# Optimization experiments

Hardware: AMD Instinct MI355X
Metric: run time of the kernel (lower is better)

The kernel has to match this reference:

```python
import jax, jax.numpy as jnp
import numpy as np

N_NODES = 50000
EPS = 1e-12  # F.normalize eps


def _gcn_layer(x, W, b, src, dst):
    # GCNConv(normalize=False): h = x @ W, then sum-aggregate messages from
    # source nodes into target nodes along edge_index, then add bias.
    h = x @ W
    agg = jax.ops.segment_sum(h[src], dst, num_segments=N_NODES)
    out = agg + b
    # F.normalize(p=2, dim=-1) then ReLU
    norm = jnp.linalg.norm(out, axis=-1, keepdims=True)
    out = out / jnp.maximum(norm, EPS)
    return jax.nn.relu(out)


def setup_inputs() -> dict:
    key = jax.random.key(0)
    ks = jax.random.split(key, 8)
    nfeat, nhid, nclass, n_edges = 128, 128, 40, 640000
    x = jax.random.normal(ks[0], (N_NODES, nfeat), dtype=jnp.float32)
    edge_index = jax.random.randint(ks[1], (2, n_edges), 0, N_NODES, dtype=jnp.int64)
    s = 1.0 / np.sqrt(nhid)
    return {
        "x": x,
        "edge_index": edge_index,
        "W1": jax.random.normal(ks[2], (nfeat, nhid), jnp.float32) * s,
        "b1": jnp.zeros((nhid,), jnp.float32),
        "W2": jax.random.normal(ks[3], (nhid, nhid), jnp.float32) * s,
        "b2": jnp.zeros((nhid,), jnp.float32),
        "W3": jax.random.normal(ks[4], (nhid, nhid), jnp.float32) * s,
        "b3": jnp.zeros((nhid,), jnp.float32),
        "W4": jax.random.normal(ks[5], (nhid, nhid), jnp.float32) * s,
        "b4": jnp.zeros((nhid,), jnp.float32),
        "Wl": jax.random.normal(ks[6], (nhid, nclass), jnp.float32) * s,
        "bl": jnp.zeros((nclass,), jnp.float32),
    }


def reference(x, edge_index, W1, b1, W2, b2, W3, b3, W4, b4, Wl, bl):
    src, dst = edge_index[0], edge_index[1]
    x1 = _gcn_layer(x, W1, b1, src, dst)
    x2 = _gcn_layer(x1, W2, b2, src, dst)
    x3 = _gcn_layer(x2, W3, b3, src, dst)
    x4 = _gcn_layer(x3, W4, b4, src, dst)
    logits = x4 @ Wl + bl
    probs = jax.nn.softmax(logits, axis=-1)
    return (logits, probs, x4)
```

## Files before the change

### kernel.cpp

```cpp
#include <hip/hip_runtime.h>
#include <hip/hip_bf16.h>
#include <hip/hip_fp16.h>
#include <math.h>

#define NFEAT 128
#define NCLASS 40

typedef __attribute__((ext_vector_type(8))) short frag_ab;
typedef __attribute__((ext_vector_type(4))) float frag_cd;

static __device__ inline unsigned short f2bf_rne(float f) {
    union { float f; unsigned u; } v;
    v.f = f;
    unsigned r = v.u + 0x7FFFu + ((v.u >> 16) & 1u);
    return (unsigned short)(r >> 16);
}
static __device__ inline float bf2f(unsigned short h) {
    union { unsigned u; float f; } v;
    v.u = ((unsigned)h) << 16;
    return v.f;
}


__global__ __launch_bounds__(256) void prep_kernel(const float* __restrict__ x,
                                                   __half* __restrict__ xh, int xc4,
                                                   int* __restrict__ cnt, int n_nodes,
                                                   const float* __restrict__ W0,
                                                   const float* __restrict__ W1,
                                                   const float* __restrict__ W2,
                                                   const float* __restrict__ W3,
                                                   short* __restrict__ whi,
                                                   short* __restrict__ wlo,
                                                   int convB, int zeroB) {
    int b = blockIdx.x;
    if (b < convB) {
        int i = b * 256 + threadIdx.x;
        if (i < xc4) {
            float4 v = ((const float4*)x)[i];
            ((__half2*)xh)[i * 2 + 0] = __floats2half2_rn(v.x, v.y);
            ((__half2*)xh)[i * 2 + 1] = __floats2half2_rn(v.z, v.w);
        }
    } else if (b < convB + zeroB) {
        int i = (b - convB) * 256 + threadIdx.x;
        if (i < n_nodes) cnt[i] = 0;
    } else {
        int wb = b - convB - zeroB;
        int layer = wb >> 3;
        const float* W = layer == 0 ? W0 : layer == 1 ? W1 : layer == 2 ? W2 : W3;
        short* h = whi + (size_t)layer * 16384;
        short* l = wlo + (size_t)layer * 16384;
        int idx = (wb & 7) * 256 + threadIdx.x;
        int lane = idx & 63;
        int t = (idx >> 6) & 7;
        int s = idx >> 9;
        int quad = lane >> 4;
        int n = lane & 15;
        int kbase = s * 32 + quad * 8;
        int col = t * 16 + n;
#pragma unroll
        for (int j = 0; j < 8; ++j) {
            float f = W[(size_t)(kbase + j) * NFEAT + col];
            unsigned short hb = f2bf_rne(f);
            unsigned short lb = f2bf_rne(f - bf2f(hb));
            h[(size_t)idx * 8 + j] = (short)hb;
            l[(size_t)idx * 8 + j] = (short)lb;
        }
    }
}


__global__ __launch_bounds__(256) void hist_kernel(const int* __restrict__ dst,
                                                   int* __restrict__ counts, int n_edges) {
    int i = blockIdx.x * 256 + threadIdx.x;
    int n4 = n_edges >> 2;
    if (i < n4) {
        int4 d = ((const int4*)dst)[i];
        atomicAdd(&counts[d.x], 1);
        atomicAdd(&counts[d.y], 1);
        atomicAdd(&counts[d.z], 1);
        atomicAdd(&counts[d.w], 1);
    }
    if (i == 0) {
        for (int e = n4 << 2; e < n_edges; ++e) atomicAdd(&counts[dst[e]], 1);
    }
}

__global__ __launch_bounds__(256) void scan1_kernel(const int* __restrict__ cnt,
                                                    int* __restrict__ excl,
                                                    int* __restrict__ bsums, int n) {
    __shared__ int sd[256];
    int t = threadIdx.x;
    int i = blockIdx.x * 256 + t;
    int v = (i < n) ? cnt[i] : 0;
    sd[t] = v;
    __syncthreads();
#pragma unroll
    for (int off = 1; off < 256; off <<= 1) {
        int tmp = (t >= off) ? sd[t - off] : 0;
        __syncthreads();
        sd[t] += tmp;
        __syncthreads();
    }
    if (i < n) excl[i] = sd[t] - v;
    if (t == 255) bsums[blockIdx.x] = sd[255];
}

__global__ __launch_bounds__(256) void scan2_kernel(int* __restrict__ bsums, int nb) {
    __shared__ int sd[256];
    int t = threadIdx.x;
    int v = (t < nb) ? bsums[t] : 0;
    sd[t] = v;
    __syncthreads();
#pragma unroll
    for (int off = 1; off < 256; off <<= 1) {
        int tmp = (t >= off) ? sd[t - off] : 0;
        __syncthreads();
        sd[t] += tmp;
        __syncthreads();
    }
    if (t < nb) bsums[t] = sd[t] - v;
    if (t == 255) bsums[nb] = sd[255];
}

__global__ __launch_bounds__(256) void scan3_kernel(const int* __restrict__ excl,
                                                    const int* __restrict__ bsums,
                                                    int* __restrict__ row_ptr,
                                                    int* __restrict__ woff, int n, int nb) {
    int i = blockIdx.x * 256 + threadIdx.x;
    if (i < n) {
        int v = excl[i] + bsums[blockIdx.x];
        row_ptr[i] = v;
        woff[i] = v;
    }
    if (i == 0) row_ptr[n] = bsums[nb];
}

__global__ __launch_bounds__(256) void scatter_kernel(const int* __restrict__ src,
                                                      const int* __restrict__ dst,
                                                      int* __restrict__ woff,
                                                      int* __restrict__ src_sorted, int n_edges) {
    int i = blockIdx.x * 256 + threadIdx.x;
    int n4 = n_edges >> 2;
    if (i < n4) {
        int4 d = ((const int4*)dst)[i];
        int4 s = ((const int4*)src)[i];
        int p0 = atomicAdd(&woff[d.x], 1);
        int p1 = atomicAdd(&woff[d.y], 1);
        int p2 = atomicAdd(&woff[d.z], 1);
        int p3 = atomicAdd(&woff[d.w], 1);
        src_sorted[p0] = s.x;
        src_sorted[p1] = s.y;
        src_sorted[p2] = s.z;
        src_sorted[p3] = s.w;
    }
    if (i == 0) {
        for (int e = n4 << 2; e < n_edges; ++e) {
            int p = atomicAdd(&woff[dst[e]], 1);
            src_sorted[p] = src[e];
        }
    }
}


__global__ __launch_bounds__(256) void gcn_fused_kernel(const __half* __restrict__ xin,
                                                        const int* __restrict__ row_ptr,
                                                        const int* __restrict__ src_sorted,
                                                        const short* __restrict__ whi,
                                                        const short* __restrict__ wlo,
                                                        const float* __restrict__ bias,
                                                        float* __restrict__ outf,
                                                        __half* __restrict__ outh, int M) {
    __shared__ float smem[64][132];
    int tid = threadIdx.x;
    int base = blockIdx.x * 64;

    {
        int c = tid & 15;
        int sub = tid >> 4;
        const uint4* xp = (const uint4*)xin;
#pragma unroll 1
        for (int p = 0; p < 4; ++p) {
            int nl = p * 16 + sub;
            int node = base + nl;
            float a[8];
#pragma unroll
            for (int i = 0; i < 8; ++i) a[i] = 0.f;
            int jb = 0, je = 0;
            if (node < M) { jb = row_ptr[node]; je = row_ptr[node + 1]; }
            int j = jb;
            for (; j + 3 < je; j += 4) {
                int s0 = src_sorted[j];
                int s1 = src_sorted[j + 1];
                int s2 = src_sorted[j + 2];
                int s3 = src_sorted[j + 3];
                uint4 r0 = xp[s0 * 16 + c];
                uint4 r1 = xp[s1 * 16 + c];
                uint4 r2 = xp[s2 * 16 + c];
                uint4 r3 = xp[s3 * 16 + c];
#pragma unroll
                for (int q = 0; q < 4; ++q) {
                    unsigned u0 = (&r0.x)[q], u1 = (&r1.x)[q], u2 = (&r2.x)[q], u3 = (&r3.x)[q];
                    float2 f0 = __half22float2(*(__half2*)&u0);
                    float2 f1 = __half22float2(*(__half2*)&u1);
                    float2 f2 = __half22float2(*(__half2*)&u2);
                    float2 f3 = __half22float2(*(__half2*)&u3);
                    a[q * 2 + 0] += f0.x + f1.x + f2.x + f3.x;
                    a[q * 2 + 1] += f0.y + f1.y + f2.y + f3.y;
                }
            }
            for (; j < je; ++j) {
                int s0 = src_sorted[j];
                uint4 r0 = xp[s0 * 16 + c];
#pragma unroll
                for (int q = 0; q < 4; ++q) {
                    unsigned u0 = (&r0.x)[q];
                    float2 f0 = __half22float2(*(__half2*)&u0);
                    a[q * 2 + 0] += f0.x;
                    a[q * 2 + 1] += f0.y;
                }
            }
            float4* wp = (float4*)&smem[nl][c * 8];
            wp[0] = make_float4(a[0], a[1], a[2], a[3]);
            wp[1] = make_float4(a[4], a[5], a[6], a[7]);
        }
    }
    __syncthreads();

    int wave = tid >> 6;
    int lane = tid & 63;
    int quad = lane >> 4;
    int n16 = lane & 15;
    int lrow = wave * 16 + n16;

    const frag_ab* WH = (const frag_ab*)whi;
    const frag_ab* WL = (const frag_ab*)wlo;

    frag_cd acc[8];
#pragma unroll
    for (int t = 0; t < 8; ++t) acc[t] = (frag_cd){0.f, 0.f, 0.f, 0.f};

#pragma unroll
    for (int s = 0; s < 4; ++s) {
        const float* ap = &smem[lrow][s * 32 + quad * 8];
        float4 v0 = *(const float4*)(ap);
        float4 v1 = *(const float4*)(ap + 4);
        float fv[8] = {v0.x, v0.y, v0.z, v0.w, v1.x, v1.y, v1.z, v1.w};
        frag_ab ah, al;
#pragma unroll
        for (int jj = 0; jj < 8; ++jj) {
            unsigned short hb = f2bf_rne(fv[jj]);
            ah[jj] = (short)hb;
            al[jj] = (short)f2bf_rne(fv[jj] - bf2f(hb));
        }
#pragma unroll
        for (int t = 0; t < 8; ++t) {
            frag_ab bh = WH[(s * 8 + t) * 64 + lane];
            frag_ab bl = WL[(s * 8 + t) * 64 + lane];
            acc[t] = __builtin_amdgcn_mfma_f32_16x16x32_bf16(ah, bh, acc[t], 0, 0, 0);
            acc[t] = __builtin_amdgcn_mfma_f32_16x16x32_bf16(ah, bl, acc[t], 0, 0, 0);
            acc[t] = __builtin_amdgcn_mfma_f32_16x16x32_bf16(al, bh, acc[t], 0, 0, 0);
        }
    }

    float ssq[4] = {0.f, 0.f, 0.f, 0.f};
#pragma unroll
    for (int t = 0; t < 8; ++t) {
        float bv = bias[t * 16 + n16];
#pragma unroll
        for (int r = 0; r < 4; ++r) {
            acc[t][r] += bv;
            ssq[r] += acc[t][r] * acc[t][r];
        }
    }
#pragma unroll
    for (int mask = 1; mask <= 8; mask <<= 1) {
#pragma unroll
        for (int r = 0; r < 4; ++r) ssq[r] += __shfl_xor(ssq[r], mask);
    }
    float inv[4];
#pragma unroll
    for (int r = 0; r < 4; ++r) inv[r] = 1.0f / fmaxf(sqrtf(ssq[r]), 1e-12f);

    int orow0 = base + wave * 16 + quad * 4;
#pragma unroll
    for (int r = 0; r < 4; ++r) {
        int orow = orow0 + r;
        if (orow < M) {
            if (outh) {
                __half* op = outh + (size_t)orow * NFEAT + n16;
#pragma unroll
                for (int t = 0; t < 8; ++t)
                    op[t * 16] = __float2half(fmaxf(acc[t][r] * inv[r], 0.f));
            } else {
                float* op = outf + (size_t)orow * NFEAT + n16;
#pragma unroll
                for (int t = 0; t < 8; ++t)
                    op[t * 16] = fmaxf(acc[t][r] * inv[r], 0.f);
            }
        }
    }
}


__global__ __launch_bounds__(256) void classifier_kernel(const float* __restrict__ x4,
                                                         const float* __restrict__ Wl,
                                                         const float* __restrict__ bl,
                                                         float* __restrict__ logits,
                                                         float* __restrict__ probs, int n_nodes) {
    int node = blockIdx.x * 256 + threadIdx.x;
    int nc = node < n_nodes ? node : n_nodes - 1;
    const float* row = x4 + (size_t)nc * NFEAT;

    float acc[NCLASS];
#pragma unroll
    for (int c = 0; c < NCLASS; ++c) acc[c] = bl[c];

    for (int k = 0; k < NFEAT; k += 4) {
        float4 a = *(const float4*)(row + k);
#pragma unroll
        for (int kk = 0; kk < 4; ++kk) {
            float av = (&a.x)[kk];
            const float* Wr = Wl + (k + kk) * NCLASS;
#pragma unroll
            for (int c = 0; c < NCLASS; ++c) acc[c] += av * Wr[c];
        }
    }

    float m = acc[0];
#pragma unroll
    for (int c = 1; c < NCLASS; ++c) m = fmaxf(m, acc[c]);
    float ex[NCLASS];
    float sum = 0.f;
#pragma unroll
    for (int c = 0; c < NCLASS; ++c) {
        ex[c] = __expf(acc[c] - m);
        sum += ex[c];
    }
    float is = 1.0f / sum;

    if (node < n_nodes) {
        float4* lo = (float4*)(logits + (size_t)node * NCLASS);
        float4* po = (float4*)(probs + (size_t)node * NCLASS);
#pragma unroll
        for (int c = 0; c < NCLASS; c += 4) {
            float4 lv, pv;
            lv.x = acc[c + 0]; lv.y = acc[c + 1]; lv.z = acc[c + 2]; lv.w = acc[c + 3];
            pv.x = ex[c + 0] * is; pv.y = ex[c + 1] * is; pv.z = ex[c + 2] * is; pv.w = ex[c + 3] * is;
            lo[c >> 2] = lv;
            po[c >> 2] = pv;
        }
    }
}


extern "C" void kernel_launch(void* const* d_in, const int* in_sizes, int n_in,
                              void* d_out, int out_size, void* d_ws, size_t ws_size,
                              hipStream_t stream) {
    const float* x  = (const float*)d_in[0];
    const int*   ei = (const int*)d_in[1];
    const float* W1 = (const float*)d_in[2];
    const float* b1 = (const float*)d_in[3];
    const float* W2 = (const float*)d_in[4];
    const float* b2 = (const float*)d_in[5];
    const float* W3 = (const float*)d_in[6];
    const float* b3 = (const float*)d_in[7];
    const float* W4 = (const float*)d_in[8];
    const float* b4 = (const float*)d_in[9];
    const float* Wl = (const float*)d_in[10];
    const float* bl = (const float*)d_in[11];

    const int n_nodes = in_sizes[0] / NFEAT;
    const int n_edges = in_sizes[1] / 2;
    const int* src = ei;
    const int* dst = ei + n_edges;

    float* out    = (float*)d_out;
    float* logits = out;
    float* probs  = out + (size_t)n_nodes * NCLASS;
    float* x4     = out + 2 * (size_t)n_nodes * NCLASS;

    char* ws = (char*)d_ws;
    size_t off = 0;
    auto wsalloc = [&](size_t bytes) -> void* {
        void* p = ws + off;
        off += (bytes + 255) & ~(size_t)255;
        return p;
    };
    __half* xh         = (__half*)wsalloc((size_t)n_nodes * NFEAT * sizeof(__half));
    __half* xh2        = (__half*)wsalloc((size_t)n_nodes * NFEAT * sizeof(__half));
    int*    row_ptr    = (int*)wsalloc(((size_t)n_nodes + 1) * sizeof(int));
    int*    woff       = (int*)wsalloc((size_t)n_nodes * sizeof(int));
    int*    cnt        = (int*)wsalloc((size_t)n_nodes * sizeof(int));
    int*    src_sorted = (int*)wsalloc((size_t)n_edges * sizeof(int));
    int     nbt        = (n_nodes + 255) / 256;
    int*    bsums      = (int*)wsalloc(((size_t)nbt + 1) * sizeof(int));
    short*  whi        = (short*)wsalloc((size_t)4 * 16384 * sizeof(short));
    short*  wlo        = (short*)wsalloc((size_t)4 * 16384 * sizeof(short));

    int xc4   = (n_nodes * NFEAT) / 4;
    int convB = (xc4 + 255) / 256;
    int zeroB = (n_nodes + 255) / 256;
    prep_kernel<<<convB + zeroB + 32, 256, 0, stream>>>(x, xh, xc4, cnt, n_nodes,
                                                        W1, W2, W3, W4, whi, wlo,
                                                        convB, zeroB);

    int e4b = ((n_edges >> 2) + 255) / 256;
    hist_kernel<<<e4b, 256, 0, stream>>>(dst, cnt, n_edges);
    scan1_kernel<<<nbt, 256, 0, stream>>>(cnt, row_ptr , bsums, n_nodes);
    scan2_kernel<<<1, 256, 0, stream>>>(bsums, nbt);
    scan3_kernel<<<nbt, 256, 0, stream>>>(row_ptr, bsums, row_ptr, woff, n_nodes, nbt);
    scatter_kernel<<<e4b, 256, 0, stream>>>(src, dst, woff, src_sorted, n_edges);

    int gb = (n_nodes + 63) / 64;
    int cb = (n_nodes + 255) / 256;

    gcn_fused_kernel<<<gb, 256, 0, stream>>>(xh,  row_ptr, src_sorted, whi + 0 * 16384, wlo + 0 * 16384, b1, nullptr, xh2, n_nodes);
    gcn_fused_kernel<<<gb, 256, 0, stream>>>(xh2, row_ptr, src_sorted, whi + 1 * 16384, wlo + 1 * 16384, b2, nullptr, xh,  n_nodes);
    gcn_fused_kernel<<<gb, 256, 0, stream>>>(xh,  row_ptr, src_sorted, whi + 2 * 16384, wlo + 2 * 16384, b3, nullptr, xh2, n_nodes);
    gcn_fused_kernel<<<gb, 256, 0, stream>>>(xh2, row_ptr, src_sorted, whi + 3 * 16384, wlo + 3 * 16384, b4, x4, nullptr, n_nodes);

    classifier_kernel<<<cb, 256, 0, stream>>>(x4, Wl, bl, logits, probs, n_nodes);
}
```

Measured before the change: 349.4 us.

## Merge histogram into prep kernel, fuse scan stages, add dynamic node scheduling

Moves the destination-degree histogram into the prep kernel and replaces the in-kernel count zeroing with a memset, which removes one launch. Scan2 is folded into scan3: every block redundantly scans the block sums in shared memory, so the single-block launch goes away. In the fused GCN kernel, each 16-lane group now takes node indices from a shared atomic counter instead of a fixed 4-node assignment, to balance uneven degrees within a block. The cost is extra shared atomics and shuffles, plus redundant scan work in each block.

New measurement: 347.8 us. No clear change (-0.5%).

```diff
diff --git a/kernel.cpp b/kernel.cpp
--- a/kernel.cpp
+++ b/kernel.cpp
@@ -24,14 +24,15 @@
 
 __global__ __launch_bounds__(256) void prep_kernel(const float* __restrict__ x,
                                                    __half* __restrict__ xh, int xc4,
-                                                   int* __restrict__ cnt, int n_nodes,
                                                    const float* __restrict__ W0,
                                                    const float* __restrict__ W1,
                                                    const float* __restrict__ W2,
                                                    const float* __restrict__ W3,
                                                    short* __restrict__ whi,
                                                    short* __restrict__ wlo,
-                                                   int convB, int zeroB) {
+                                                   const int* __restrict__ dst,
+                                                   int* __restrict__ cnt, int n_edges,
+                                                   int convB) {
     int b = blockIdx.x;
     if (b < convB) {
         int i = b * 256 + threadIdx.x;
@@ -40,11 +41,8 @@
             ((__half2*)xh)[i * 2 + 0] = __floats2half2_rn(v.x, v.y);
             ((__half2*)xh)[i * 2 + 1] = __floats2half2_rn(v.z, v.w);
         }
-    } else if (b < convB + zeroB) {
-        int i = (b - convB) * 256 + threadIdx.x;
-        if (i < n_nodes) cnt[i] = 0;
-    } else {
-        int wb = b - convB - zeroB;
+    } else if (b < convB + 32) {
+        int wb = b - convB;
         int layer = wb >> 3;
         const float* W = layer == 0 ? W0 : layer == 1 ? W1 : layer == 2 ? W2 : W3;
         short* h = whi + (size_t)layer * 16384;
@@ -65,25 +63,23 @@
             h[(size_t)idx * 8 + j] = (short)hb;
             l[(size_t)idx * 8 + j] = (short)lb;
         }
-    }
-}
-
-
-__global__ __launch_bounds__(256) void hist_kernel(const int* __restrict__ dst,
-                                                   int* __restrict__ counts, int n_edges) {
-    int i = blockIdx.x * 256 + threadIdx.x;
-    int n4 = n_edges >> 2;
-    if (i < n4) {
-        int4 d = ((const int4*)dst)[i];
-        atomicAdd(&counts[d.x], 1);
-        atomicAdd(&counts[d.y], 1);
-        atomicAdd(&counts[d.z], 1);
-        atomicAdd(&counts[d.w], 1);
-    }
-    if (i == 0) {
-        for (int e = n4 << 2; e < n_edges; ++e) atomicAdd(&counts[dst[e]], 1);
-    }
-}
+    } else {
+        int hb = b - convB - 32;
+        int i = hb * 256 + threadIdx.x;
+        int n4 = n_edges >> 2;
+        if (i < n4) {
+            int4 d = ((const int4*)dst)[i];
+            atomicAdd(&cnt[d.x], 1);
+            atomicAdd(&cnt[d.y], 1);
+            atomicAdd(&cnt[d.z], 1);
+            atomicAdd(&cnt[d.w], 1);
+        }
+        if (hb == 0 && threadIdx.x == 0) {
+            for (int e = n4 << 2; e < n_edges; ++e) atomicAdd(&cnt[dst[e]], 1);
+        }
+    }
+}
+
 
 __global__ __launch_bounds__(256) void scan1_kernel(const int* __restrict__ cnt,
                                                     int* __restrict__ excl,
@@ -105,8 +101,12 @@
     if (t == 255) bsums[blockIdx.x] = sd[255];
 }
 
-__global__ __launch_bounds__(256) void scan2_kernel(int* __restrict__ bsums, int nb) {
+__global__ __launch_bounds__(256) void scan3_kernel(const int* __restrict__ excl,
+                                                    const int* __restrict__ bsums,
+                                                    int* __restrict__ row_ptr,
+                                                    int* __restrict__ woff, int n, int nb) {
     __shared__ int sd[256];
+    __shared__ int off_s, tot_s;
     int t = threadIdx.x;
     int v = (t < nb) ? bsums[t] : 0;
     sd[t] = v;
@@ -118,21 +118,18 @@
         sd[t] += tmp;
         __syncthreads();
     }
-    if (t < nb) bsums[t] = sd[t] - v;
-    if (t == 255) bsums[nb] = sd[255];
-}
-
-__global__ __launch_bounds__(256) void scan3_kernel(const int* __restrict__ excl,
-                                                    const int* __restrict__ bsums,
-                                                    int* __restrict__ row_ptr,
-                                                    int* __restrict__ woff, int n, int nb) {
-    int i = blockIdx.x * 256 + threadIdx.x;
+    if (t == 0) {
+        off_s = (blockIdx.x > 0) ? sd[blockIdx.x - 1] : 0;
+        tot_s = sd[255];
+    }
+    __syncthreads();
+    int i = blockIdx.x * 256 + t;
     if (i < n) {
-        int v = excl[i] + bsums[blockIdx.x];
-        row_ptr[i] = v;
-        woff[i] = v;
-    }
-    if (i == 0) row_ptr[n] = bsums[nb];
+        int val = excl[i] + off_s;
+        row_ptr[i] = val;
+        woff[i] = val;
+    }
+    if (i == 0) row_ptr[n] = tot_s;
 }
 
 __global__ __launch_bounds__(256) void scatter_kernel(const int* __restrict__ src,
@@ -171,16 +168,21 @@
                                                         float* __restrict__ outf,
                                                         __half* __restrict__ outh, int M) {
     __shared__ float smem[64][132];
+    __shared__ int ctr;
     int tid = threadIdx.x;
     int base = blockIdx.x * 64;
+    if (tid == 0) ctr = 0;
+    __syncthreads();
 
     {
         int c = tid & 15;
-        int sub = tid >> 4;
+        int lane = tid & 63;
         const uint4* xp = (const uint4*)xin;
-#pragma unroll 1
-        for (int p = 0; p < 4; ++p) {
-            int nl = p * 16 + sub;
+        for (;;) {
+            int nl = 0;
+            if ((lane & 15) == 0) nl = atomicAdd(&ctr, 1);
+            nl = __shfl(nl, lane & 48);
+            if (nl >= 64) break;
             int node = base + nl;
             float a[8];
 #pragma unroll
@@ -397,17 +399,16 @@
     short*  whi        = (short*)wsalloc((size_t)4 * 16384 * sizeof(short));
     short*  wlo        = (short*)wsalloc((size_t)4 * 16384 * sizeof(short));
 
+    hipMemsetAsync(cnt, 0, (size_t)n_nodes * sizeof(int), stream);
+
     int xc4   = (n_nodes * NFEAT) / 4;
     int convB = (xc4 + 255) / 256;
-    int zeroB = (n_nodes + 255) / 256;
-    prep_kernel<<<convB + zeroB + 32, 256, 0, stream>>>(x, xh, xc4, cnt, n_nodes,
-                                                        W1, W2, W3, W4, whi, wlo,
-                                                        convB, zeroB);
-
-    int e4b = ((n_edges >> 2) + 255) / 256;
-    hist_kernel<<<e4b, 256, 0, stream>>>(dst, cnt, n_edges);
+    int e4b   = ((n_edges >> 2) + 255) / 256;
+    prep_kernel<<<convB + 32 + e4b, 256, 0, stream>>>(x, xh, xc4,
+                                                      W1, W2, W3, W4, whi, wlo,
+                                                      dst, cnt, n_edges, convB);
+
     scan1_kernel<<<nbt, 256, 0, stream>>>(cnt, row_ptr , bsums, n_nodes);
-    scan2_kernel<<<1, 256, 0, stream>>>(bsums, nbt);
     scan3_kernel<<<nbt, 256, 0, stream>>>(row_ptr, bsums, row_ptr, woff, n_nodes, nbt);
     scatter_kernel<<<e4b, 256, 0, stream>>>(src, dst, woff, src_sorted, n_edges);
 
```
